# Optimization experiments

Measured on AMD Instinct MI355X. Metric: run time of the kernel, lower is better.

Reference implementation:

```python
import jax, jax.numpy as jnp
import numpy as np

H, W = 14, 14
MIN_RATIO, MAX_RATIO = 0.25, 1.0
GLOBAL_RATIO = 0.5


def setup_inputs() -> dict:
    key = jax.random.key(0)
    motion = jax.random.uniform(key, (512, 1, 224, 224), dtype=jnp.float32)
    return {"motion_magnitude": motion, "num_tokens": 6272}


def reference(motion_magnitude, num_tokens):
    B, C, Hin, Win = motion_magnitude.shape
    # adaptive_avg_pool2d to (14,14): input dims are exact multiples -> block mean
    fh, fw = Hin // H, Win // W
    motion_resized = motion_magnitude.reshape(B, C, H, fh, W, fw).mean(axis=(3, 5))  # (B,1,H,W)
    m_min = motion_resized.min()
    m_max = motion_resized.max()
    motion_normalized = (motion_resized - m_min) / (m_max - m_min + 1e-6)
    importance_scores = motion_normalized[:, 0]  # (B,H,W)
    compression_ratio = MIN_RATIO + (MAX_RATIO - MIN_RATIO) * importance_scores
    current_avg = compression_ratio.mean()
    scale = GLOBAL_RATIO / (current_avg + 1e-6)
    scaled = jnp.clip(compression_ratio * scale, MIN_RATIO, MAX_RATIO)
    compression_ratio = jnp.where(current_avg > 0, scaled, compression_ratio)

    # --- vectorized get_merge_indices (replaces double Python loop) ---
    ratio_flat = compression_ratio.reshape(B, H * W)
    tpp = num_tokens // (H * W)  # tokens per patch
    k = jnp.clip(jnp.round(ratio_flat * tpp).astype(jnp.int32), 1, tpp)  # (B,HW)
    # keep first k tokens inside each patch's contiguous block of tpp tokens
    within = jnp.arange(tpp, dtype=jnp.int32)  # (tpp,)
    mask = (within[None, None, :] < k[:, :, None]).astype(jnp.float32)  # (B,HW,tpp)
    merge_mask = mask.reshape(B, H * W * tpp)
    if H * W * tpp < num_tokens:  # pad remainder with zeros (kept at 0 in original)
        merge_mask = jnp.pad(merge_mask, ((0, 0), (0, num_tokens - H * W * tpp)))
    return compression_ratio, importance_scores, merge_mask
```

## Files before the change

kernel.cpp:

```cpp
#include <hip/hip_runtime.h>
#include <math.h>

#define HW2   196
#define IMG   224
#define IMG2  (224*224)
#define NBLK1 3584

__global__ __launch_bounds__(256) void k_patch_mean(const float* __restrict__ in,
                                                    float* __restrict__ resized,
                                                    float* __restrict__ pmin,
                                                    float* __restrict__ pmax,
                                                    double* __restrict__ psum,
                                                    int npair) {
    int wid  = threadIdx.x >> 6;
    int lane = threadIdx.x & 63;
    int row  = lane >> 2;
    int c4   = lane & 3;
    int ngroups = (npair + 3) / 4;

    float  mn = INFINITY, mx = -INFINITY;
    double sm = 0.0;

    for (int g = blockIdx.x; g < ngroups; g += gridDim.x) {
        int p = g * 4 + wid;
        if (p < npair) {
            int b   = p / HW2;
            int rem = p - b * HW2;
            int py  = rem / 14;
            int px  = rem - py * 14;
            const float4* src = (const float4*)(in + (size_t)b * IMG2
                                                  + (size_t)(py * 16 + row) * IMG
                                                  + px * 16) + c4;
            float4 v = *src;
            float s = (v.x + v.y) + (v.z + v.w);
            #pragma unroll
            for (int off = 32; off; off >>= 1) s += __shfl_xor(s, off, 64);
            if (lane == 0) {
                float mean = s * (1.0f / 256.0f);
                resized[p] = mean;
                mn = fminf(mn, mean);
                mx = fmaxf(mx, mean);
                sm += (double)mean;
            }
        }
    }

    __shared__ float  smn[4], smx[4];
    __shared__ double ssm[4];
    if (lane == 0) { smn[wid] = mn; smx[wid] = mx; ssm[wid] = sm; }
    __syncthreads();
    if (threadIdx.x == 0) {
        pmin[blockIdx.x] = fminf(fminf(smn[0], smn[1]), fminf(smn[2], smn[3]));
        pmax[blockIdx.x] = fmaxf(fmaxf(smx[0], smx[1]), fmaxf(smx[2], smx[3]));
        psum[blockIdx.x] = ssm[0] + ssm[1] + ssm[2] + ssm[3];
    }
}

__global__ __launch_bounds__(256) void k_output(const float* __restrict__ resized,
                                                const float* __restrict__ pmin,
                                                const float* __restrict__ pmax,
                                                const double* __restrict__ psum,
                                                int nblk1,
                                                float* __restrict__ out,
                                                int npair, int tpp, int num_tokens) {
    int t = threadIdx.x;
    float  mn = INFINITY, mx = -INFINITY;
    double s  = 0.0;
    for (int i = t; i < nblk1; i += 256) {
        mn = fminf(mn, pmin[i]);
        mx = fmaxf(mx, pmax[i]);
        s += psum[i];
    }
    #pragma unroll
    for (int off = 32; off; off >>= 1) {
        mn = fminf(mn, __shfl_xor(mn, off, 64));
        mx = fmaxf(mx, __shfl_xor(mx, off, 64));
        s += __shfl_xor(s, off, 64);
    }
    __shared__ float  smn[4], smx[4];
    __shared__ double ssm[4];
    __shared__ float  sc3[3];
    int wid = t >> 6, lane = t & 63;
    if (lane == 0) { smn[wid] = mn; smx[wid] = mx; ssm[wid] = s; }
    __syncthreads();
    if (t == 0) {
        mn = fminf(fminf(smn[0], smn[1]), fminf(smn[2], smn[3]));
        mx = fmaxf(fmaxf(smx[0], smx[1]), fmaxf(smx[2], smx[3]));
        s  = ssm[0] + ssm[1] + ssm[2] + ssm[3];
        float denom = __fadd_rn(__fsub_rn(mx, mn), 1e-6f);
        double mean     = s / (double)npair;
        double avg_norm = (mean - (double)mn) / (double)denom;
        double cur_avg  = 0.25 + 0.75 * avg_norm;
        sc3[0] = mn;
        sc3[1] = denom;
        sc3[2] = (float)(0.5 / (cur_avg + 1e-6));
    }
    __syncthreads();
    float fmn = sc3[0], fden = sc3[1], fscale = sc3[2];

    int base = blockIdx.x * 256;
    int g = base + t;
    __shared__ int      kk[256];
    __shared__ unsigned kbase[256];
    int k = 0;
    unsigned kb = 0;
    if (g < npair) {
        float r = resized[g];
        float norm   = __fdiv_rn(__fsub_rn(r, fmn), fden);
        float ratio0 = __fadd_rn(0.25f, __fmul_rn(0.75f, norm));
        float sc     = __fmul_rn(ratio0, fscale);
        float ratio  = fminf(fmaxf(sc, 0.25f), 1.0f);
        k = (int)rintf(__fmul_rn(ratio, (float)tpp));
        k = min(max(k, 1), tpp);
        out[g]         = ratio;
        out[npair + g] = norm;
        unsigned b = (unsigned)g / HW2;
        unsigned p = (unsigned)g - b * HW2;
        kb = b * (unsigned)num_tokens + p * (unsigned)tpp;
    }
    kk[t]    = k;
    kbase[t] = kb;
    __syncthreads();

    float* mask = out + 2 * (size_t)npair;
    int nprs = min(256, npair - base);
    if ((tpp & 3) == 0) {
        int tq = tpp >> 2;
        int total4 = nprs * tq;
        for (int i = t; i < total4; i += 256) {
            int pr = (unsigned)i / (unsigned)tq;
            int wi = (i - pr * tq) * 4;
            int kv = kk[pr];
            float4 m;
            m.x = (wi     < kv) ? 1.0f : 0.0f;
            m.y = (wi + 1 < kv) ? 1.0f : 0.0f;
            m.z = (wi + 2 < kv) ? 1.0f : 0.0f;
            m.w = (wi + 3 < kv) ? 1.0f : 0.0f;
            *(float4*)(mask + (size_t)kbase[pr] + wi) = m;
        }
    } else {
        int total = nprs * tpp;
        for (int i = t; i < total; i += 256) {
            int pr = (unsigned)i / (unsigned)tpp;
            int wi = i - pr * tpp;
            mask[(size_t)kbase[pr] + wi] = (wi < kk[pr]) ? 1.0f : 0.0f;
        }
    }
}

__global__ void k_pad(float* __restrict__ mask, int B, int num_tokens, int used) {
    int per = num_tokens - used;
    int idx = blockIdx.x * 256 + threadIdx.x;
    int tot = B * per;
    if (idx < tot) {
        int b = idx / per;
        int j = idx - b * per;
        mask[(size_t)b * num_tokens + used + j] = 0.0f;
    }
}

extern "C" void kernel_launch(void* const* d_in, const int* in_sizes, int n_in,
                              void* d_out, int out_size, void* d_ws, size_t ws_size,
                              hipStream_t stream) {
    const float* motion = (const float*)d_in[0];
    int nelem = in_sizes[0];
    int B     = nelem / IMG2;
    int npair = B * HW2;
    int num_tokens = (out_size - 2 * npair) / B;
    int tpp   = num_tokens / HW2;

    float* resized = (float*)d_ws;
    size_t off = ((size_t)npair * sizeof(float) + 7) & ~(size_t)7;
    double* psum = (double*)((char*)d_ws + off);
    float*  pmin = (float*)(psum + NBLK1);
    float*  pmax = pmin + NBLK1;

    int ngroups = (npair + 3) / 4;
    int nb1 = min(NBLK1, ngroups);
    hipLaunchKernelGGL(k_patch_mean, dim3(nb1), dim3(256), 0, stream,
                       motion, resized, pmin, pmax, psum, npair);

    int nb2 = (npair + 255) / 256;
    hipLaunchKernelGGL(k_output, dim3(nb2), dim3(256), 0, stream,
                       resized, pmin, pmax, psum, nb1,
                       (float*)d_out, npair, tpp, num_tokens);

    int used = HW2 * tpp;
    if (used < num_tokens) {
        int tot = B * (num_tokens - used);
        hipLaunchKernelGGL(k_pad, dim3((tot + 255) / 256), dim3(256), 0, stream,
                           (float*)d_out + 2 * (size_t)npair, B, num_tokens, used);
    }
}
```

Measured before the change: 31.25 us.

## Batch eight patches per wavefront with independent loads and interleaved shuffles

Result: slower. 33.30 us (+6.6%).

```diff
diff --git a/kernel.cpp b/kernel.cpp
--- a/kernel.cpp
+++ b/kernel.cpp
@@ -4,7 +4,8 @@
 #define HW2   196
 #define IMG   224
 #define IMG2  (224*224)
-#define NBLK1 3584
+#define PPW   8
+#define PPB   32
 
 __global__ __launch_bounds__(256) void k_patch_mean(const float* __restrict__ in,
                                                     float* __restrict__ resized,
@@ -12,17 +13,18 @@
                                                     float* __restrict__ pmax,
                                                     double* __restrict__ psum,
                                                     int npair) {
-    int wid  = threadIdx.x >> 6;
-    int lane = threadIdx.x & 63;
-    int row  = lane >> 2;
-    int c4   = lane & 3;
-    int ngroups = (npair + 3) / 4;
-
-    float  mn = INFINITY, mx = -INFINITY;
-    double sm = 0.0;
-
-    for (int g = blockIdx.x; g < ngroups; g += gridDim.x) {
-        int p = g * 4 + wid;
+    const int t    = threadIdx.x;
+    const int wid  = t >> 6;
+    const int lane = t & 63;
+    const int row  = lane >> 2;
+    const int c4   = lane & 3;
+    const int p0   = blockIdx.x * PPB + wid * PPW;
+
+    float s[PPW];
+    #pragma unroll
+    for (int k = 0; k < PPW; ++k) {
+        int p = p0 + k;
+        float4 v = make_float4(0.f, 0.f, 0.f, 0.f);
         if (p < npair) {
             int b   = p / HW2;
             int rem = p - b * HW2;
@@ -31,16 +33,38 @@
             const float4* src = (const float4*)(in + (size_t)b * IMG2
                                                   + (size_t)(py * 16 + row) * IMG
                                                   + px * 16) + c4;
-            float4 v = *src;
-            float s = (v.x + v.y) + (v.z + v.w);
+            v = *src;
+        }
+        s[k] = (v.x + v.y) + (v.z + v.w);
+    }
+
+    #pragma unroll
+    for (int off = 32; off; off >>= 1) {
+        #pragma unroll
+        for (int k = 0; k < PPW; ++k) s[k] += __shfl_xor(s[k], off, 64);
+    }
+
+    float  mn = INFINITY, mx = -INFINITY;
+    double sm = 0.0;
+    if (lane == 0) {
+        float m[PPW];
+        #pragma unroll
+        for (int k = 0; k < PPW; ++k) m[k] = s[k] * (1.0f / 256.0f);
+        if (p0 + PPW <= npair) {
+            *(float4*)(resized + p0)     = make_float4(m[0], m[1], m[2], m[3]);
+            *(float4*)(resized + p0 + 4) = make_float4(m[4], m[5], m[6], m[7]);
             #pragma unroll
-            for (int off = 32; off; off >>= 1) s += __shfl_xor(s, off, 64);
-            if (lane == 0) {
-                float mean = s * (1.0f / 256.0f);
-                resized[p] = mean;
-                mn = fminf(mn, mean);
-                mx = fmaxf(mx, mean);
-                sm += (double)mean;
+            for (int k = 0; k < PPW; ++k) {
+                mn = fminf(mn, m[k]);
+                mx = fmaxf(mx, m[k]);
+                sm += (double)m[k];
+            }
+        } else {
+            for (int k = 0; k < PPW && p0 + k < npair; ++k) {
+                resized[p0 + k] = m[k];
+                mn = fminf(mn, m[k]);
+                mx = fmaxf(mx, m[k]);
+                sm += (double)m[k];
             }
         }
     }
@@ -49,7 +73,7 @@
     __shared__ double ssm[4];
     if (lane == 0) { smn[wid] = mn; smx[wid] = mx; ssm[wid] = sm; }
     __syncthreads();
-    if (threadIdx.x == 0) {
+    if (t == 0) {
         pmin[blockIdx.x] = fminf(fminf(smn[0], smn[1]), fminf(smn[2], smn[3]));
         pmax[blockIdx.x] = fmaxf(fmaxf(smx[0], smx[1]), fmaxf(smx[2], smx[3]));
         psum[blockIdx.x] = ssm[0] + ssm[1] + ssm[2] + ssm[3];
@@ -96,7 +120,7 @@
         sc3[2] = (float)(0.5 / (cur_avg + 1e-6));
     }
     __syncthreads();
-    float fmn = sc3[0], fden = sc3[1], fscale = sc3[2];
+    const float fmn = sc3[0], fden = sc3[1], fscale = sc3[2];
 
     int base = blockIdx.x * 256;
     int g = base + t;
@@ -169,14 +193,14 @@
     int num_tokens = (out_size - 2 * npair) / B;
     int tpp   = num_tokens / HW2;
 
+    int nb1 = (npair + PPB - 1) / PPB;
+
     float* resized = (float*)d_ws;
     size_t off = ((size_t)npair * sizeof(float) + 7) & ~(size_t)7;
     double* psum = (double*)((char*)d_ws + off);
-    float*  pmin = (float*)(psum + NBLK1);
-    float*  pmax = pmin + NBLK1;
-
-    int ngroups = (npair + 3) / 4;
-    int nb1 = min(NBLK1, ngroups);
+    float*  pmin = (float*)(psum + nb1);
+    float*  pmax = pmin + nb1;
+
     hipLaunchKernelGGL(k_patch_mean, dim3(nb1), dim3(256), 0, stream,
                        motion, resized, pmin, pmax, psum, npair);
 
```
